# Performance work log

Measured on AMD Instinct MI355X. Metric: run time of the kernel, lower is better.

The kernel has to match this reference:

```python
import jax, jax.numpy as jnp
import numpy as np

N_NODES = 100000
N_FEAT = 512
N_CLASS = 64
N_EDGES = 3200000
NLAYERS = 2


def setup_inputs() -> dict:
    key = jax.random.key(0)
    k1, k2, k3, k4, k5 = jax.random.split(key, 5)
    x = jax.random.normal(k1, (N_NODES, N_FEAT), dtype=jnp.float32)
    # xavier_uniform on weight.T => bound = sqrt(6/(fan_in+fan_out))
    bound = float(np.sqrt(6.0 / (N_FEAT + N_CLASS)))
    weight = jax.random.uniform(k2, (N_FEAT, N_CLASS), dtype=jnp.float32,
                                minval=-bound, maxval=bound)
    bias = jnp.zeros((N_CLASS,), dtype=jnp.float32)
    edge_row = jax.random.randint(k3, (N_EDGES,), 0, N_NODES, dtype=jnp.int32)
    edge_col = jax.random.randint(k4, (N_EDGES,), 0, N_NODES, dtype=jnp.int32)
    edge_val = jax.random.uniform(k5, (N_EDGES,), dtype=jnp.float32)
    return {"x": x, "weight": weight, "bias": bias,
            "edge_row": edge_row, "edge_col": edge_col, "edge_val": edge_val,
            "nlayers": NLAYERS}


def _spmm(edge_row, edge_col, edge_val, h):
    # out[r] = sum_{e: row[e]==r} val[e] * h[col[e]]   (adj @ h)
    msgs = edge_val[:, None] * h[edge_col]  # [E, C]
    return jax.ops.segment_sum(msgs, edge_row, num_segments=h.shape[0])


def reference(x, weight, bias, edge_row, edge_col, edge_val, nlayers):
    h = x @ weight                      # [N, C] dense GEMM
    for _ in range(nlayers):            # repeated sparse propagation
        h = _spmm(edge_row, edge_col, edge_val, h)
    h = h + bias
    return jax.nn.log_softmax(h, axis=1)
```

## Files before the change

kernel.cpp:

```cpp
#include <hip/hip_runtime.h>
#include <hip/hip_bf16.h>

constexpr int NROWS = 100000;
constexpr int K     = 512;
constexpr int C     = 64;
constexpr int E     = 3200000;

constexpr int NBK     = 256;
constexpr int BROWS   = 391;
constexpr int BSTRIDE = 13824;
constexpr int CHUNK   = 4096;

typedef __attribute__((ext_vector_type(8))) short bf16x8;
typedef __attribute__((ext_vector_type(4))) float f32x4;

__global__ __launch_bounds__(256) void prep_w(const float* __restrict__ w,
                                              unsigned short* __restrict__ wfrag) {
  int idx = blockIdx.x * 256 + threadIdx.x;
  if (idx >= K * C) return;
  int k = idx >> 6, n = idx & 63;
  float v = w[idx];
  unsigned u = __float_as_uint(v);
  unsigned short hi = (unsigned short)(u >> 16);
  float rem = v - __uint_as_float(u & 0xFFFF0000u);
  unsigned lu = __float_as_uint(rem);
  unsigned short lo = (unsigned short)((lu + 0x7FFF + ((lu >> 16) & 1)) >> 16);
  int ks = k >> 5, kr = k & 31, g = kr >> 3, j = kr & 7;
  int lane = (g << 4) | (n & 15), nt = n >> 4;
  size_t base = ((size_t)(ks * 4 + nt)) * 1024 + lane * 8 + j;
  wfrag[base]       = hi;
  wfrag[base + 512] = lo;
}

__device__ inline bf16x8 pack_bf16x8(unsigned p0, unsigned p1, unsigned p2, unsigned p3) {
  union { int4 i; bf16x8 b; } u;
  u.i = make_int4((int)p0, (int)p1, (int)p2, (int)p3);
  return u.b;
}

__global__ __launch_bounds__(256) void gemm_mfma(const float* __restrict__ x,
                                                 const unsigned short* __restrict__ wfrag,
                                                 float* __restrict__ h) {
  const int t    = threadIdx.x;
  const int lane = t & 63;
  const int lr   = lane & 15;
  const int g    = lane >> 4;
  const int row0 = blockIdx.x * 64 + (t >> 6) * 16;

  int gr = row0 + lr;
  if (gr >= NROWS) gr = NROWS - 1;
  const float* xr = x + (size_t)gr * K;

  f32x4 acc0 = {0.f, 0.f, 0.f, 0.f};
  f32x4 acc1 = {0.f, 0.f, 0.f, 0.f};
  f32x4 acc2 = {0.f, 0.f, 0.f, 0.f};
  f32x4 acc3 = {0.f, 0.f, 0.f, 0.f};

  for (int ks = 0; ks < K / 32; ++ks) {
    const float* xp = xr + ks * 32 + g * 8;
    float4 A0 = *(const float4*)xp;
    float4 A1 = *(const float4*)(xp + 4);
    unsigned u0 = __float_as_uint(A0.x), u1 = __float_as_uint(A0.y);
    unsigned u2 = __float_as_uint(A0.z), u3 = __float_as_uint(A0.w);
    unsigned u4 = __float_as_uint(A1.x), u5 = __float_as_uint(A1.y);
    unsigned u6 = __float_as_uint(A1.z), u7 = __float_as_uint(A1.w);
    bf16x8 ah = pack_bf16x8((u1 & 0xFFFF0000u) | (u0 >> 16),
                            (u3 & 0xFFFF0000u) | (u2 >> 16),
                            (u5 & 0xFFFF0000u) | (u4 >> 16),
                            (u7 & 0xFFFF0000u) | (u6 >> 16));
    float r0 = A0.x - __uint_as_float(u0 & 0xFFFF0000u);
    float r1 = A0.y - __uint_as_float(u1 & 0xFFFF0000u);
    float r2 = A0.z - __uint_as_float(u2 & 0xFFFF0000u);
    float r3 = A0.w - __uint_as_float(u3 & 0xFFFF0000u);
    float r4 = A1.x - __uint_as_float(u4 & 0xFFFF0000u);
    float r5 = A1.y - __uint_as_float(u5 & 0xFFFF0000u);
    float r6 = A1.z - __uint_as_float(u6 & 0xFFFF0000u);
    float r7 = A1.w - __uint_as_float(u7 & 0xFFFF0000u);
    unsigned l0 = __float_as_uint(r0), l1 = __float_as_uint(r1);
    unsigned l2 = __float_as_uint(r2), l3 = __float_as_uint(r3);
    unsigned l4 = __float_as_uint(r4), l5 = __float_as_uint(r5);
    unsigned l6 = __float_as_uint(r6), l7 = __float_as_uint(r7);
    l0 = (l0 + 0x7FFF + ((l0 >> 16) & 1)) >> 16;
    l1 = (l1 + 0x7FFF + ((l1 >> 16) & 1)) >> 16;
    l2 = (l2 + 0x7FFF + ((l2 >> 16) & 1)) >> 16;
    l3 = (l3 + 0x7FFF + ((l3 >> 16) & 1)) >> 16;
    l4 = (l4 + 0x7FFF + ((l4 >> 16) & 1)) >> 16;
    l5 = (l5 + 0x7FFF + ((l5 >> 16) & 1)) >> 16;
    l6 = (l6 + 0x7FFF + ((l6 >> 16) & 1)) >> 16;
    l7 = (l7 + 0x7FFF + ((l7 >> 16) & 1)) >> 16;
    bf16x8 al = pack_bf16x8((l1 << 16) | l0, (l3 << 16) | l2,
                            (l5 << 16) | l4, (l7 << 16) | l6);

    const unsigned short* wp = wfrag + (size_t)ks * 4096;
#pragma unroll
    for (int nt = 0; nt < 4; ++nt) {
      bf16x8 bh = *(const bf16x8*)(wp + nt * 1024 + lane * 8);
      bf16x8 bl = *(const bf16x8*)(wp + nt * 1024 + 512 + lane * 8);
      f32x4& acc = (nt == 0) ? acc0 : (nt == 1) ? acc1 : (nt == 2) ? acc2 : acc3;
      acc = __builtin_amdgcn_mfma_f32_16x16x32_bf16(ah, bh, acc, 0, 0, 0);
      acc = __builtin_amdgcn_mfma_f32_16x16x32_bf16(al, bh, acc, 0, 0, 0);
      acc = __builtin_amdgcn_mfma_f32_16x16x32_bf16(ah, bl, acc, 0, 0, 0);
    }
  }

#pragma unroll
  for (int i = 0; i < 4; ++i) {
    int r = row0 + g * 4 + i;
    if (r < NROWS) {
      float* hp = h + (size_t)r * C + lr;
      hp[0]  = acc0[i];
      hp[16] = acc1[i];
      hp[32] = acc2[i];
      hp[48] = acc3[i];
    }
  }
}

__global__ __launch_bounds__(256) void gemm64(const float* __restrict__ x,
                                              const float* __restrict__ w,
                                              float* __restrict__ h) {
  __shared__ float xs[128][65];
  __shared__ float ws[64][64];
  const int t    = threadIdx.x;
  const int cg   = (t & 15) * 4;
  const int rg   = (t >> 4) * 8;
  const int row0 = blockIdx.x * 128;

  float acc[8][4] = {};

  for (int k0 = 0; k0 < K; k0 += 64) {
    {
      const float4* wg  = (const float4*)(w + (size_t)k0 * C);
      float4*       wsv = (float4*)&ws[0][0];
#pragma unroll
      for (int i = 0; i < 4; ++i) wsv[t + 256 * i] = wg[t + 256 * i];
    }
#pragma unroll
    for (int i = 0; i < 8; ++i) {
      int idx = t + 256 * i;
      int r   = idx >> 4;
      int kk  = (idx & 15) * 4;
      int gr  = row0 + r;
      if (gr >= NROWS) gr = NROWS - 1;
      float4 v = *(const float4*)(x + (size_t)gr * K + k0 + kk);
      xs[r][kk]     = v.x;
      xs[r][kk + 1] = v.y;
      xs[r][kk + 2] = v.z;
      xs[r][kk + 3] = v.w;
    }
    __syncthreads();

#pragma unroll 8
    for (int kk = 0; kk < 64; ++kk) {
      float4 wv = *(const float4*)&ws[kk][cg];
      float xr[8];
#pragma unroll
      for (int i = 0; i < 8; ++i) xr[i] = xs[rg + i][kk];
#pragma unroll
      for (int i = 0; i < 8; ++i) {
        acc[i][0] += xr[i] * wv.x;
        acc[i][1] += xr[i] * wv.y;
        acc[i][2] += xr[i] * wv.z;
        acc[i][3] += xr[i] * wv.w;
      }
    }
    __syncthreads();
  }

#pragma unroll
  for (int i = 0; i < 8; ++i) {
    int gr = row0 + rg + i;
    if (gr < NROWS) {
      float4 v = {acc[i][0], acc[i][1], acc[i][2], acc[i][3]};
      *(float4*)(h + (size_t)gr * C + cg) = v;
    }
  }
}

__global__ __launch_bounds__(256) void init_bcur(int* __restrict__ bcur) {
  int t = threadIdx.x;
  if (t < NBK) bcur[t] = t * BSTRIDE;
}

__device__ inline int wave_incl_scan(int v, int lane) {
#pragma unroll
  for (int off = 1; off < 64; off <<= 1) {
    int t = __shfl_up(v, off, 64);
    if (lane >= off) v += t;
  }
  return v;
}

__global__ __launch_bounds__(256) void bin_by_row(const int* __restrict__ row,
                                                  const int* __restrict__ col,
                                                  const float* __restrict__ val,
                                                  int* bcur,
                                                  int2* __restrict__ binned) {
  __shared__ int hist[NBK];
  __shared__ int hcur[NBK];
  __shared__ int gbase[NBK];
  __shared__ int wt[4];
  __shared__ int2 lrec[CHUNK];
  __shared__ unsigned char lb[CHUNK];

  const int t  = threadIdx.x;
  const int e0 = blockIdx.x * CHUNK;
  const int n  = min(CHUNK, E - e0);

  hist[t] = 0;
  __syncthreads();

  int pb[16], px[16], pv[16];
#pragma unroll
  for (int i = 0; i < 16; ++i) {
    int e = e0 + 256 * i + t;
    pb[i] = -1;
    if (e < E) {
      int r = __builtin_nontemporal_load(row + e);
      int c = __builtin_nontemporal_load(col + e);
      float v = __builtin_nontemporal_load(val + e);
      int b = r / BROWS;
      pb[i] = b;
      px[i] = (r - b * BROWS) | (c << 9);
      pv[i] = __float_as_int(v);
      atomicAdd(&hist[b], 1);
    }
  }
  __syncthreads();

  {
    int lane = t & 63, wv = t >> 6;
    int d = hist[t];
    int inc = wave_incl_scan(d, lane);
    if (lane == 63) wt[wv] = inc;
    __syncthreads();
    int woff = 0;
    for (int w = 0; w < wv; ++w) woff += wt[w];
    hcur[t] = woff + inc - d;
  }

  {
    int cnt = hist[t];
    int gb  = cnt ? atomicAdd(&bcur[t], cnt) : 0;
    gbase[t] = gb - hcur[t];
  }
  __syncthreads();

#pragma unroll
  for (int i = 0; i < 16; ++i) {
    if (pb[i] >= 0) {
      int l = atomicAdd(&hcur[pb[i]], 1);
      lrec[l] = make_int2(px[i], pv[i]);
      lb[l]   = (unsigned char)pb[i];
    }
  }
  __syncthreads();

  for (int l = t; l < n; l += 256) {
    int b = lb[l];
    binned[gbase[b] + l] = lrec[l];
  }
}

__global__ __launch_bounds__(1024) void sort_bucket(const int2* __restrict__ binned,
                                                    const int* __restrict__ bcur,
                                                    int2* __restrict__ pack,
                                                    int* __restrict__ rs,
                                                    int* __restrict__ deg) {
  __shared__ int2 rec[BSTRIDE];
  __shared__ int  hist[BROWS];
  __shared__ int  excl[BROWS];
  __shared__ int  wt[16];

  const int b    = blockIdx.x;
  const int t    = threadIdx.x;
  const int base = b * BSTRIDE;
  const int cnt  = bcur[b] - base;

  for (int i = t; i < cnt; i += 1024) rec[i] = binned[base + i];
  for (int i = t; i < BROWS; i += 1024) hist[i] = 0;
  __syncthreads();

  for (int i = t; i < cnt; i += 1024) atomicAdd(&hist[rec[i].x & 511], 1);
  __syncthreads();

  {
    int lane = t & 63, wv = t >> 6;
    int d = (t < BROWS) ? hist[t] : 0;
    int inc = wave_incl_scan(d, lane);
    if (lane == 63) wt[wv] = inc;
    __syncthreads();
    int woff = 0;
    for (int w = 0; w < wv; ++w) woff += wt[w];
    if (t < BROWS) excl[t] = woff + inc - d;
  }
  __syncthreads();

  const int row0 = b * BROWS;
  for (int i = t; i < BROWS; i += 1024) {
    int gr = row0 + i;
    if (gr < NROWS) {
      rs[gr]  = base + excl[i];
      deg[gr] = hist[i];
    }
  }
  __syncthreads();

  for (int i = t; i < cnt; i += 1024) {
    int2 p    = rec[i];
    int local = p.x & 511;
    int off   = atomicAdd(&excl[local], 1);
    pack[base + off] = make_int2(((unsigned)p.x) >> 9, p.y);
  }
}

__global__ __launch_bounds__(256) void spmm_pull(const int* __restrict__ rs,
                                                 const int* __restrict__ deg,
                                                 const int2* __restrict__ pack,
                                                 const float* __restrict__ hin,
                                                 float* __restrict__ hout) {
  int r = blockIdx.x * 4 + (threadIdx.x >> 6);
  if (r >= NROWS) return;
  int lane  = threadIdx.x & 63;
  int start = rs[r], end = start + deg[r];
  float acc = 0.f;
  for (int base = start; base < end; base += 64) {
    int idx = base + lane;
    int2 p  = (idx < end) ? pack[idx] : make_int2(0, 0);
    int n   = min(64, end - base);
    int nn  = (n + 3) & ~3;
    for (int j = 0; j < nn; j += 4) {
      int   c0 = __shfl(p.x, j, 64),     c1 = __shfl(p.x, j + 1, 64);
      int   c2 = __shfl(p.x, j + 2, 64), c3 = __shfl(p.x, j + 3, 64);
      float v0 = __int_as_float(__shfl(p.y, j, 64));
      float v1 = __int_as_float(__shfl(p.y, j + 1, 64));
      float v2 = __int_as_float(__shfl(p.y, j + 2, 64));
      float v3 = __int_as_float(__shfl(p.y, j + 3, 64));
      float g0 = hin[(size_t)c0 * C + lane];
      float g1 = hin[(size_t)c1 * C + lane];
      float g2 = hin[(size_t)c2 * C + lane];
      float g3 = hin[(size_t)c3 * C + lane];
      acc += v0 * g0; acc += v1 * g1; acc += v2 * g2; acc += v3 * g3;
    }
  }
  hout[(size_t)r * C + lane] = acc;
}

__global__ __launch_bounds__(256) void spmm_atomic(const int* __restrict__ row,
                                                   const int* __restrict__ col,
                                                   const float* __restrict__ val,
                                                   const float* __restrict__ hin,
                                                   float* hout) {
  int e = blockIdx.x * 4 + (threadIdx.x >> 6);
  if (e >= E) return;
  int   c  = threadIdx.x & 63;
  int   r  = row[e];
  int   cl = col[e];
  float v  = val[e];
  atomicAdd(&hout[(size_t)r * C + c], v * hin[(size_t)cl * C + c]);
}

__global__ __launch_bounds__(256) void bias_lsm(const float* __restrict__ h,
                                                const float* __restrict__ bias,
                                                float* __restrict__ out) {
  int r = blockIdx.x * 4 + (threadIdx.x >> 6);
  if (r >= NROWS) return;
  int   c = threadIdx.x & 63;
  float v = h[(size_t)r * C + c] + bias[c];

  float m = v;
#pragma unroll
  for (int off = 32; off; off >>= 1) m = fmaxf(m, __shfl_xor(m, off, 64));
  float ex = __expf(v - m);
  float s  = ex;
#pragma unroll
  for (int off = 32; off; off >>= 1) s += __shfl_xor(s, off, 64);

  out[(size_t)r * C + c] = v - m - __logf(s);
}

extern "C" void kernel_launch(void* const* d_in, const int* in_sizes, int n_in,
                              void* d_out, int out_size, void* d_ws, size_t ws_size,
                              hipStream_t stream) {
  const float* x    = (const float*)d_in[0];
  const float* w    = (const float*)d_in[1];
  const float* bias = (const float*)d_in[2];
  const int*   erow = (const int*)d_in[3];
  const int*   ecol = (const int*)d_in[4];
  const float* eval = (const float*)d_in[5];

  float* out = (float*)d_out;

  const size_t hbytes = (size_t)NROWS * C * sizeof(float);
  const size_t bbytes = (size_t)NBK * BSTRIDE * sizeof(int2);
  const size_t wfbytes = (size_t)K * C * 2 * sizeof(unsigned short);
  char* ws = (char*)d_ws;

  const int nblk_bin = (E + CHUNK - 1) / CHUNK;

  const size_t regA = (bbytes > hbytes) ? bbytes : hbytes;

  size_t need = regA + bbytes  + (size_t)NROWS * 8 + (size_t)NBK * 4
              + wfbytes + 8192;

  if (ws_size >= need) {
    char* p = ws;
    char* regA_p = p;                 p += regA;
    int2*  pack  = (int2*)p;          p += bbytes;
    int*   rs    = (int*)p;           p += (size_t)NROWS * 4;
    int*   deg   = (int*)p;           p += (size_t)NROWS * 4;
    int*   bcur  = (int*)p;           p += (size_t)NBK * 4;
    unsigned short* wfrag = (unsigned short*)p;

    int2*  binned = (int2*)regA_p;
    float* h0     = (float*)regA_p;
    float* hA     = out;

    prep_w<<<(K * C + 255) / 256, 256, 0, stream>>>(w, wfrag);

    init_bcur<<<1, 256, 0, stream>>>(bcur);
    bin_by_row<<<nblk_bin, 256, 0, stream>>>(erow, ecol, eval, bcur, binned);
    sort_bucket<<<NBK, 1024, 0, stream>>>(binned, bcur, pack, rs, deg);

    gemm_mfma<<<(NROWS + 63) / 64, 256, 0, stream>>>(x, wfrag, h0);

    spmm_pull<<<(NROWS + 3) / 4, 256, 0, stream>>>(rs, deg, pack, h0, hA);
    spmm_pull<<<(NROWS + 3) / 4, 256, 0, stream>>>(rs, deg, pack, hA, h0);

    bias_lsm<<<(NROWS + 3) / 4, 256, 0, stream>>>(h0, bias, out);
  } else {
    float* h0 = (float*)ws;
    float* hA = out;
    gemm64<<<(NROWS + 127) / 128, 256, 0, stream>>>(x, w, h0);
    hipMemsetAsync(hA, 0, hbytes, stream);
    spmm_atomic<<<(E + 3) / 4, 256, 0, stream>>>(erow, ecol, eval, h0, hA);
    hipMemsetAsync(h0, 0, hbytes, stream);
    spmm_atomic<<<(E + 3) / 4, 256, 0, stream>>>(erow, ecol, eval, hA, h0);
    bias_lsm<<<(NROWS + 3) / 4, 256, 0, stream>>>(h0, bias, out);
  }
}
```

Before: 612.8 us.

## Store intermediate features in fp16, fuse bias+log_softmax into last SpMM, finer row buckets

The GEMM output and the intermediate SpMM result are now stored as half precision, which halves the bytes moved by the gathers in the pull-based SpMM. Each wave now handles two edges per step, with each half-wave loading half2 pairs, and the halves are combined with a cross-lane shuffle. The second SpMM adds the bias and computes log_softmax inline, which removes a separate kernel and one full-precision round trip. Row binning is changed to 512 buckets of 196 rows, so sort_bucket needs less shared memory and has more blocks. The cost is fp16 rounding of the intermediates, which could affect accuracy.

```diff
diff --git a/kernel.cpp b/kernel.cpp
--- a/kernel.cpp
+++ b/kernel.cpp
@@ -1,14 +1,15 @@
 #include <hip/hip_runtime.h>
 #include <hip/hip_bf16.h>
+#include <hip/hip_fp16.h>
 
 constexpr int NROWS = 100000;
 constexpr int K     = 512;
 constexpr int C     = 64;
 constexpr int E     = 3200000;
 
-constexpr int NBK     = 256;
-constexpr int BROWS   = 391;
-constexpr int BSTRIDE = 13824;
+constexpr int NBK     = 512;
+constexpr int BROWS   = 196;
+constexpr int BSTRIDE = 7232;
 constexpr int CHUNK   = 4096;
 
 typedef __attribute__((ext_vector_type(8))) short bf16x8;
@@ -40,7 +41,7 @@
 
 __global__ __launch_bounds__(256) void gemm_mfma(const float* __restrict__ x,
                                                  const unsigned short* __restrict__ wfrag,
-                                                 float* __restrict__ h) {
+                                                 __half* __restrict__ h16) {
   const int t    = threadIdx.x;
   const int lane = t & 63;
   const int lr   = lane & 15;
@@ -107,11 +108,11 @@
   for (int i = 0; i < 4; ++i) {
     int r = row0 + g * 4 + i;
     if (r < NROWS) {
-      float* hp = h + (size_t)r * C + lr;
-      hp[0]  = acc0[i];
-      hp[16] = acc1[i];
-      hp[32] = acc2[i];
-      hp[48] = acc3[i];
+      __half* hp = h16 + (size_t)r * C + lr;
+      hp[0]  = __float2half(acc0[i]);
+      hp[16] = __float2half(acc1[i]);
+      hp[32] = __float2half(acc2[i]);
+      hp[48] = __float2half(acc3[i]);
     }
   }
 }
@@ -177,7 +178,7 @@
   }
 }
 
-__global__ __launch_bounds__(256) void init_bcur(int* __restrict__ bcur) {
+__global__ __launch_bounds__(512) void init_bcur(int* __restrict__ bcur) {
   int t = threadIdx.x;
   if (t < NBK) bcur[t] = t * BSTRIDE;
 }
@@ -201,13 +202,13 @@
   __shared__ int gbase[NBK];
   __shared__ int wt[4];
   __shared__ int2 lrec[CHUNK];
-  __shared__ unsigned char lb[CHUNK];
+  __shared__ unsigned short lb[CHUNK];
 
   const int t  = threadIdx.x;
   const int e0 = blockIdx.x * CHUNK;
   const int n  = min(CHUNK, E - e0);
 
-  hist[t] = 0;
+  hist[t] = 0; hist[t + 256] = 0;
   __syncthreads();
 
   int pb[16], px[16], pv[16];
@@ -221,7 +222,7 @@
       float v = __builtin_nontemporal_load(val + e);
       int b = r / BROWS;
       pb[i] = b;
-      px[i] = (r - b * BROWS) | (c << 9);
+      px[i] = (r - b * BROWS) | (c << 8);
       pv[i] = __float_as_int(v);
       atomicAdd(&hist[b], 1);
     }
@@ -229,20 +230,25 @@
   __syncthreads();
 
   {
+    int a  = hist[2 * t];
+    int b2 = hist[2 * t + 1];
+    int s  = a + b2;
     int lane = t & 63, wv = t >> 6;
-    int d = hist[t];
-    int inc = wave_incl_scan(d, lane);
+    int inc = wave_incl_scan(s, lane);
     if (lane == 63) wt[wv] = inc;
     __syncthreads();
     int woff = 0;
     for (int w = 0; w < wv; ++w) woff += wt[w];
-    hcur[t] = woff + inc - d;
-  }
-
-  {
-    int cnt = hist[t];
-    int gb  = cnt ? atomicAdd(&bcur[t], cnt) : 0;
-    gbase[t] = gb - hcur[t];
+    int excl = woff + inc - s;
+    hcur[2 * t]     = excl;
+    hcur[2 * t + 1] = excl + a;
+  }
+  __syncthreads();
+
+  for (int i = t; i < NBK; i += 256) {
+    int cnt = hist[i];
+    int gb  = cnt ? atomicAdd(&bcur[i], cnt) : 0;
+    gbase[i] = gb - hcur[i];
   }
   __syncthreads();
 
@@ -251,7 +257,7 @@
     if (pb[i] >= 0) {
       int l = atomicAdd(&hcur[pb[i]], 1);
       lrec[l] = make_int2(px[i], pv[i]);
-      lb[l]   = (unsigned char)pb[i];
+      lb[l]   = (unsigned short)pb[i];
     }
   }
   __syncthreads();
@@ -281,7 +287,7 @@
   for (int i = t; i < BROWS; i += 1024) hist[i] = 0;
   __syncthreads();
 
-  for (int i = t; i < cnt; i += 1024) atomicAdd(&hist[rec[i].x & 511], 1);
+  for (int i = t; i < cnt; i += 1024) atomicAdd(&hist[rec[i].x & 255], 1);
   __syncthreads();
 
   {
@@ -308,22 +314,27 @@
 
   for (int i = t; i < cnt; i += 1024) {
     int2 p    = rec[i];
-    int local = p.x & 511;
+    int local = p.x & 255;
     int off   = atomicAdd(&excl[local], 1);
-    pack[base + off] = make_int2(((unsigned)p.x) >> 9, p.y);
-  }
-}
-
-__global__ __launch_bounds__(256) void spmm_pull(const int* __restrict__ rs,
-                                                 const int* __restrict__ deg,
-                                                 const int2* __restrict__ pack,
-                                                 const float* __restrict__ hin,
-                                                 float* __restrict__ hout) {
+    pack[base + off] = make_int2(((unsigned)p.x) >> 8, p.y);
+  }
+}
+
+template <int MODE>
+__global__ __launch_bounds__(256) void spmm16(const int* __restrict__ rs,
+                                              const int* __restrict__ deg,
+                                              const int2* __restrict__ pack,
+                                              const __half* __restrict__ hin,
+                                              const float* __restrict__ bias,
+                                              __half* __restrict__ hout16,
+                                              float* __restrict__ outf) {
   int r = blockIdx.x * 4 + (threadIdx.x >> 6);
   if (r >= NROWS) return;
-  int lane  = threadIdx.x & 63;
+  const int lane = threadIdx.x & 63;
+  const int hf   = lane >> 5;
+  const int m    = lane & 31;
   int start = rs[r], end = start + deg[r];
-  float acc = 0.f;
+  float ax = 0.f, ay = 0.f;
   for (int base = start; base < end; base += 64) {
     int idx = base + lane;
     int2 p  = (idx < end) ? pack[idx] : make_int2(0, 0);
@@ -336,14 +347,39 @@
       float v1 = __int_as_float(__shfl(p.y, j + 1, 64));
       float v2 = __int_as_float(__shfl(p.y, j + 2, 64));
       float v3 = __int_as_float(__shfl(p.y, j + 3, 64));
-      float g0 = hin[(size_t)c0 * C + lane];
-      float g1 = hin[(size_t)c1 * C + lane];
-      float g2 = hin[(size_t)c2 * C + lane];
-      float g3 = hin[(size_t)c3 * C + lane];
-      acc += v0 * g0; acc += v1 * g1; acc += v2 * g2; acc += v3 * g3;
-    }
-  }
-  hout[(size_t)r * C + lane] = acc;
+      int   cA = hf ? c1 : c0;  float vA = hf ? v1 : v0;
+      int   cB = hf ? c3 : c2;  float vB = hf ? v3 : v2;
+      __half2 gA = *(const __half2*)(hin + (size_t)cA * C + 2 * m);
+      __half2 gB = *(const __half2*)(hin + (size_t)cB * C + 2 * m);
+      float2 fA = __half22float2(gA);
+      float2 fB = __half22float2(gB);
+      ax = fmaf(vA, fA.x, ax); ay = fmaf(vA, fA.y, ay);
+      ax = fmaf(vB, fB.x, ax); ay = fmaf(vB, fB.y, ay);
+    }
+  }
+  ax += __shfl_xor(ax, 32, 64);
+  ay += __shfl_xor(ay, 32, 64);
+
+  if (MODE == 0) {
+    if (hf == 0) {
+      __half2 o = __floats2half2_rn(ax, ay);
+      *(__half2*)(hout16 + (size_t)r * C + 2 * m) = o;
+    }
+  } else {
+    float2 bb = *(const float2*)(bias + 2 * m);
+    float v0 = ax + bb.x, v1 = ay + bb.y;
+    float mx = fmaxf(v0, v1);
+#pragma unroll
+    for (int off = 16; off; off >>= 1) mx = fmaxf(mx, __shfl_xor(mx, off, 64));
+    float s = __expf(v0 - mx) + __expf(v1 - mx);
+#pragma unroll
+    for (int off = 16; off; off >>= 1) s += __shfl_xor(s, off, 64);
+    float ls = __logf(s);
+    if (hf == 0) {
+      float2 o = {v0 - mx - ls, v1 - mx - ls};
+      *(float2*)(outf + (size_t)r * C + 2 * m) = o;
+    }
+  }
 }
 
 __global__ __launch_bounds__(256) void spmm_atomic(const int* __restrict__ row,
@@ -391,14 +427,15 @@
 
   float* out = (float*)d_out;
 
-  const size_t hbytes = (size_t)NROWS * C * sizeof(float);
-  const size_t bbytes = (size_t)NBK * BSTRIDE * sizeof(int2);
+  const size_t hbytes  = (size_t)NROWS * C * sizeof(float);
+  const size_t h16b    = (size_t)NROWS * C * sizeof(__half);
+  const size_t bbytes  = (size_t)NBK * BSTRIDE * sizeof(int2);
   const size_t wfbytes = (size_t)K * C * 2 * sizeof(unsigned short);
   char* ws = (char*)d_ws;
 
   const int nblk_bin = (E + CHUNK - 1) / CHUNK;
 
-  const size_t regA = (bbytes > hbytes) ? bbytes : hbytes;
+  const size_t regA = (bbytes > 2 * h16b) ? bbytes : 2 * h16b;
 
   size_t need = regA + bbytes  + (size_t)NROWS * 8 + (size_t)NBK * 4
               + wfbytes + 8192;
@@ -412,22 +449,22 @@
     int*   bcur  = (int*)p;           p += (size_t)NBK * 4;
     unsigned short* wfrag = (unsigned short*)p;
 
-    int2*  binned = (int2*)regA_p;
-    float* h0     = (float*)regA_p;
-    float* hA     = out;
+    int2*   binned = (int2*)regA_p;
+    __half* h16    = (__half*)regA_p;
+    __half* hA16   = (__half*)(regA_p + h16b);
 
     prep_w<<<(K * C + 255) / 256, 256, 0, stream>>>(w, wfrag);
 
-    init_bcur<<<1, 256, 0, stream>>>(bcur);
+    init_bcur<<<1, 512, 0, stream>>>(bcur);
     bin_by_row<<<nblk_bin, 256, 0, stream>>>(erow, ecol, eval, bcur, binned);
     sort_bucket<<<NBK, 1024, 0, stream>>>(binned, bcur, pack, rs, deg);
 
-    gemm_mfma<<<(NROWS + 63) / 64, 256, 0, stream>>>(x, wfrag, h0);
-
-    spmm_pull<<<(NROWS + 3) / 4, 256, 0, stream>>>(rs, deg, pack, h0, hA);
-    spmm_pull<<<(NROWS + 3) / 4, 256, 0, stream>>>(rs, deg, pack, hA, h0);
-
-    bias_lsm<<<(NROWS + 3) / 4, 256, 0, stream>>>(h0, bias, out);
+    gemm_mfma<<<(NROWS + 63) / 64, 256, 0, stream>>>(x, wfrag, h16);
+
+    spmm16<0><<<(NROWS + 3) / 4, 256, 0, stream>>>(rs, deg, pack, h16, nullptr,
+                                                   hA16, nullptr);
+    spmm16<1><<<(NROWS + 3) / 4, 256, 0, stream>>>(rs, deg, pack, hA16, bias,
+                                                   nullptr, out);
   } else {
     float* h0 = (float*)ws;
     float* hA = out;
```

Result: faster. 569.5 us (-7.1%).
